# Performance work log

Hardware: AMD Instinct MI355X
Metric: run time of the kernel (lower is better)

## Reference

```python
import jax, jax.numpy as jnp
import numpy as np

N_NODES = 50000

def setup_inputs() -> dict:
    key = jax.random.key(0)
    k1, k2, k3, k4, k5, k6 = jax.random.split(key, 6)
    T, D, N, E = 10000, 128, N_NODES, 800000
    impact = jax.random.normal(k1, (T, D), dtype=jnp.float32)
    W = jax.random.normal(k2, (D, D), dtype=jnp.float32)
    M = jax.random.normal(k3, (D, D), dtype=jnp.float32)
    node_ids = jax.random.randint(k4, (N,), 0, T, dtype=jnp.int64)
    neighbor_ids = jax.random.randint(k5, (E,), 0, T, dtype=jnp.int64)
    neighbor_segments = jnp.sort(jax.random.randint(k6, (E,), 0, N, dtype=jnp.int64))
    return {"impact": impact, "W": W, "M": M, "node_ids": node_ids,
            "neighbor_ids": neighbor_ids, "neighbor_segments": neighbor_segments}

def reference(impact, W, M, node_ids, neighbor_ids, neighbor_segments):
    # Per node i (type k_i): s_i = relu(W @ h[k_i] + sum_{j in N(i)} M @ h[type_j])
    # result = softmax(sum_i s_i) over the D feature axis.
    self_feats = impact[node_ids]                          # (N, D) gather
    neigh_feats = impact[neighbor_ids]                     # (E, D) gather
    neigh_sum = jax.ops.segment_sum(neigh_feats, neighbor_segments,
                                    num_segments=N_NODES)  # (N, D) scatter-add
    pre = self_feats @ W.T + neigh_sum @ M.T               # (N, D)
    result = jnp.sum(jax.nn.relu(pre), axis=0)             # (D,)
    return jax.nn.softmax(result, axis=0)
```

## Files before the change

### kernel.cpp

```cpp
#include <hip/hip_runtime.h>
#include <hip/hip_fp16.h>

#define DDIM 128
#define ACC_BLOCKS 2048
#define NWALK (ACC_BLOCKS * 4)
#define RED_BLOCKS 64

typedef unsigned int uint;
typedef unsigned short ushort;
typedef __attribute__((ext_vector_type(8))) short bf16x8;
typedef __attribute__((ext_vector_type(4))) float f32x4;

static __device__ __forceinline__ ushort f2bf(float x) {
    uint u = __float_as_uint(x);
    u += 0x7fffu + ((u >> 16) & 1u);
    return (ushort)(u >> 16);
}

__global__ __launch_bounds__(256) void prep(
    const int* __restrict__ segs,
    const int* __restrict__ node_ids,
    const int* __restrict__ neighbor_ids,
    int* __restrict__ rowptr,
    int* __restrict__ items,
    int* __restrict__ done,
    int N, int E, int whoff, int mhoff)
{
    const int x = blockIdx.x * blockDim.x + threadIdx.x;
    if (x == 0) *done = 0;
    if (x >= E) return;

    const int sc = segs[x];
    const int sp = (x == 0) ? -1 : segs[x - 1];
    const int sn = (x + 1 < E) ? segs[x + 1] : N;

    items[x + sc + 1] = (mhoff + neighbor_ids[x] * 256) | ((sn != sc) ? (int)0x80000000 : 0);

    for (int i = sp + 1; i <= sc; ++i) {
        rowptr[i] = x;
        items[x + i] = (whoff + node_ids[i] * 256) | ((i < sc) ? (int)0x80000000 : 0);
    }
    if (x == E - 1) {
        for (int i = sc + 1; i <= N; ++i) {
            rowptr[i] = E;
            if (i < N) items[E + i] = (whoff + node_ids[i] * 256) | (int)0x80000000;
        }
#pragma unroll
        for (int q = 0; q < 32; ++q) items[N + E + q] = whoff;
    }
}

static __device__ __forceinline__ bf16x8 load_frag8(const float* base) {
    const float4 p = *reinterpret_cast<const float4*>(base);
    const float4 q = *reinterpret_cast<const float4*>(base + 4);
    bf16x8 f;
    f[0] = (short)f2bf(p.x); f[1] = (short)f2bf(p.y);
    f[2] = (short)f2bf(p.z); f[3] = (short)f2bf(p.w);
    f[4] = (short)f2bf(q.x); f[5] = (short)f2bf(q.y);
    f[6] = (short)f2bf(q.z); f[7] = (short)f2bf(q.w);
    return f;
}

__global__ __launch_bounds__(256) void precompute_mfma(
    const float* __restrict__ impact,
    const float* __restrict__ W,
    const float* __restrict__ Mm,
    __half* __restrict__ WhH,
    __half* __restrict__ MhH,
    const int* __restrict__ rowptr,
    int* __restrict__ wstart,
    int T, int N, int K)
{
    const int gid = blockIdx.x * 256 + threadIdx.x;
    if (gid <= NWALK) {
        const int t = (int)(((long long)gid * K) / NWALK);
        int lo = 0, hi = N;
        while (lo < hi) {
            const int mid = (lo + hi) >> 1;
            if (rowptr[mid] + mid < t) lo = mid + 1; else hi = mid;
        }
        wstart[gid] = rowptr[lo] + lo;
    }

    const int lane = threadIdx.x & 63;
    const int wv   = threadIdx.x >> 6;
    const int t0   = blockIdx.x * 32;
    const int r16  = lane & 15;
    const int kg   = lane >> 4;

    bf16x8 A[2][4];
#pragma unroll
    for (int rt = 0; rt < 2; ++rt) {
        int t = t0 + rt * 16 + r16;
        if (t >= T) t = T - 1;
        const float* abase = impact + (size_t)t * DDIM + kg * 8;
#pragma unroll
        for (int k0i = 0; k0i < 4; ++k0i)
            A[rt][k0i] = load_frag8(abase + k0i * 32);
    }

#pragma unroll
    for (int dti = 0; dti < 2; ++dti) {
        const int d0 = (wv * 2 + dti) * 16;
#pragma unroll
        for (int m = 0; m < 2; ++m) {
            const float* mat = (m == 0) ? W : Mm;
            __half* out = (m == 0) ? WhH : MhH;
            const float* bbase = mat + (size_t)(d0 + r16) * DDIM + kg * 8;
            f32x4 acc0 = {0.f, 0.f, 0.f, 0.f};
            f32x4 acc1 = {0.f, 0.f, 0.f, 0.f};
#pragma unroll
            for (int k0i = 0; k0i < 4; ++k0i) {
                const bf16x8 b = load_frag8(bbase + k0i * 32);
                acc0 = __builtin_amdgcn_mfma_f32_16x16x32_bf16(A[0][k0i], b, acc0, 0, 0, 0);
                acc1 = __builtin_amdgcn_mfma_f32_16x16x32_bf16(A[1][k0i], b, acc1, 0, 0, 0);
            }
            const int dcol = d0 + r16;
#pragma unroll
            for (int r = 0; r < 4; ++r) {
                const int tr0 = t0 + kg * 4 + r;
                const int tr1 = tr0 + 16;
                if (tr0 < T) out[(size_t)tr0 * DDIM + dcol] = __float2half(acc0[r]);
                if (tr1 < T) out[(size_t)tr1 * DDIM + dcol] = __float2half(acc1[r]);
            }
        }
    }
}

__global__ __launch_bounds__(256, 8) void accumulate_items(
    const char* __restrict__ tab,
    const int* __restrict__ items,
    const int* __restrict__ wstart,
    float* __restrict__ partials)
{
    const int lane = threadIdx.x & 63;
    const int wv   = __builtin_amdgcn_readfirstlane(threadIdx.x >> 6);
    const int w    = blockIdx.x * 4 + wv;

    const uint lb = (uint)lane << 2;

    const __half2 zero2 = __floats2half2_rn(0.f, 0.f);
    __half2 cc = zero2;
    float a0 = 0.f, a1 = 0.f;

    int k = __builtin_amdgcn_readfirstlane(wstart[w]);
    const int kend = __builtin_amdgcn_readfirstlane(wstart[w + 1]);

#define GATH(IW) (*reinterpret_cast<const __half2*>(tab + (((uint)(IW)) & 0x7fffffffu) + lb))
#define ACC(IW, V) { \
    cc = __hadd2(cc, V); \
    if ((IW) < 0) { \
        const float2 f = __half22float2(cc); \
        a0 += fmaxf(f.x, 0.f); a1 += fmaxf(f.y, 0.f); \
        cc = zero2; \
    } }
#define LOADI(Pa, Pb, Pc, Pd, kk) { \
    Pa = *reinterpret_cast<const int4*>(items + (kk)); \
    Pb = *reinterpret_cast<const int4*>(items + (kk) + 4); \
    Pc = *reinterpret_cast<const int4*>(items + (kk) + 8); \
    Pd = *reinterpret_cast<const int4*>(items + (kk) + 12); }
#define GATHER16(V, Pa, Pb, Pc, Pd) { \
    V[0] = GATH(Pa.x);  V[1] = GATH(Pa.y);  V[2]  = GATH(Pa.z);  V[3]  = GATH(Pa.w); \
    V[4] = GATH(Pb.x);  V[5] = GATH(Pb.y);  V[6]  = GATH(Pb.z);  V[7]  = GATH(Pb.w); \
    V[8] = GATH(Pc.x);  V[9] = GATH(Pc.y);  V[10] = GATH(Pc.z);  V[11] = GATH(Pc.w); \
    V[12] = GATH(Pd.x); V[13] = GATH(Pd.y); V[14] = GATH(Pd.z);  V[15] = GATH(Pd.w); }
#define ACC16(V, Pa, Pb, Pc, Pd) { \
    ACC(Pa.x, V[0]);  ACC(Pa.y, V[1]);  ACC(Pa.z, V[2]);   ACC(Pa.w, V[3]); \
    ACC(Pb.x, V[4]);  ACC(Pb.y, V[5]);  ACC(Pb.z, V[6]);   ACC(Pb.w, V[7]); \
    ACC(Pc.x, V[8]);  ACC(Pc.y, V[9]);  ACC(Pc.z, V[10]);  ACC(Pc.w, V[11]); \
    ACC(Pd.x, V[12]); ACC(Pd.y, V[13]); ACC(Pd.z, V[14]);  ACC(Pd.w, V[15]); }

    while (k < kend && (k & 15)) {
        const int iw = items[k];
        const __half2 v = GATH(iw);
        ACC(iw, v);
        ++k;
    }

    if (k + 32 <= kend) {
        int4 Aa, Ab, Ac, Ad, Ba, Bb, Bc, Bd;
        __half2 u[16], v[16];
        LOADI(Aa, Ab, Ac, Ad, k);
        GATHER16(u, Aa, Ab, Ac, Ad);
        LOADI(Ba, Bb, Bc, Bd, k + 16);
        k += 32;
        for (;;) {
            GATHER16(v, Ba, Bb, Bc, Bd);
            ACC16(u, Aa, Ab, Ac, Ad);
            if (k + 16 <= kend) { LOADI(Aa, Ab, Ac, Ad, k); k += 16; }
            else { ACC16(v, Ba, Bb, Bc, Bd); break; }
            GATHER16(u, Aa, Ab, Ac, Ad);
            ACC16(v, Ba, Bb, Bc, Bd);
            if (k + 16 <= kend) { LOADI(Ba, Bb, Bc, Bd, k); k += 16; }
            else { ACC16(u, Aa, Ab, Ac, Ad); break; }
        }
    }
    while (k < kend) {
        const int iw = items[k];
        const __half2 v = GATH(iw);
        ACC(iw, v);
        ++k;
    }

    {
        const float2 f = __half22float2(cc);
        a0 += fmaxf(f.x, 0.f);
        a1 += fmaxf(f.y, 0.f);
    }

    __shared__ float red[4][DDIM];
    red[wv][lane * 2 + 0] = a0;
    red[wv][lane * 2 + 1] = a1;
    __syncthreads();
    const int tid = threadIdx.x;
    if (tid < DDIM) {
        partials[(size_t)blockIdx.x * DDIM + tid] =
            red[0][tid] + red[1][tid] + red[2][tid] + red[3][tid];
    }
}

__global__ __launch_bounds__(256) void reduce_softmax(
    const float* __restrict__ partials, float* __restrict__ out2,
    float* __restrict__ out, int* __restrict__ done, int nb)
{
    const int tid = threadIdx.x;
    const int d = tid & (DDIM - 1);
    const int h = tid >> 7;
    {
        const int rows = nb / RED_BLOCKS;
        const int r0 = blockIdx.x * rows;
        float s = 0.f;
        for (int r = r0 + h; r < r0 + rows; r += 2)
            s += partials[(size_t)r * DDIM + d];
        __shared__ float red[2][DDIM];
        red[h][d] = s;
        __syncthreads();
        if (tid < DDIM)
            out2[(size_t)blockIdx.x * DDIM + tid] = red[0][tid] + red[1][tid];
    }
    __threadfence();
    __shared__ int isLast;
    if (tid == 0) {
        const int v = atomicAdd(done, 1);
        isLast = (v == RED_BLOCKS - 1) ? 1 : 0;
    }
    __syncthreads();
    if (!isLast) return;
    __threadfence();

    float s = 0.f;
    for (int b = h; b < RED_BLOCKS; b += 2)
        s += out2[(size_t)b * DDIM + d];
    __shared__ float r2[2][DDIM];
    r2[h][d] = s;
    __syncthreads();

    __shared__ float vec[DDIM];
    __shared__ float tmp[DDIM];
    if (tid < DDIM) { const float v = r2[0][tid] + r2[1][tid]; vec[tid] = v; tmp[tid] = v; }
    __syncthreads();
    for (int o = 64; o > 0; o >>= 1) {
        if (tid < o) tmp[tid] = fmaxf(tmp[tid], tmp[tid + o]);
        __syncthreads();
    }
    const float mx = tmp[0];
    __syncthreads();
    float ev = 0.f;
    if (tid < DDIM) { ev = expf(vec[tid] - mx); tmp[tid] = ev; }
    __syncthreads();
    for (int o = 64; o > 0; o >>= 1) {
        if (tid < o) tmp[tid] += tmp[tid + o];
        __syncthreads();
    }
    if (tid < DDIM) out[tid] = ev / tmp[0];
}

extern "C" void kernel_launch(void* const* d_in, const int* in_sizes, int n_in,
                              void* d_out, int out_size, void* d_ws, size_t ws_size,
                              hipStream_t stream) {
    const float* impact        = (const float*)d_in[0];
    const float* W             = (const float*)d_in[1];
    const float* Mm            = (const float*)d_in[2];
    const int*   node_ids      = (const int*)d_in[3];
    const int*   neighbor_ids  = (const int*)d_in[4];
    const int*   neighbor_segs = (const int*)d_in[5];

    const int T = in_sizes[0] / DDIM;
    const int N = in_sizes[3];
    const int E = in_sizes[4];
    const int K = N + E;

    char* ws = (char*)d_ws;
    size_t off = 0;
    const int whoff = (int)off;
    __half* WhH = (__half*)(ws + off);  off += (size_t)T * DDIM * sizeof(__half);
    const int mhoff = (int)off;
    __half* MhH = (__half*)(ws + off);  off += (size_t)T * DDIM * sizeof(__half);
    float* partials = (float*)(ws + off); off += (size_t)ACC_BLOCKS * DDIM * sizeof(float);
    float* part2    = (float*)(ws + off); off += (size_t)RED_BLOCKS * DDIM * sizeof(float);
    int*   rowptr   = (int*)(ws + off);   off += (size_t)(N + 1) * sizeof(int);
    int*   done     = (int*)(ws + off);   off += 256;
    off = (off + 255) & ~(size_t)255;
    int*   items    = (int*)(ws + off);   off += (size_t)(K + 32) * sizeof(int);
    int*   wstart   = (int*)(ws + off);   off += (size_t)(NWALK + 1) * sizeof(int);
    float* outf     = (float*)d_out;

    prep<<<(E + 255) / 256, 256, 0, stream>>>(
        neighbor_segs, node_ids, neighbor_ids, rowptr, items, done, N, E, whoff, mhoff);
    precompute_mfma<<<(T + 31) / 32, 256, 0, stream>>>(
        impact, W, Mm, WhH, MhH, rowptr, wstart, T, N, K);
    accumulate_items<<<ACC_BLOCKS, 256, 0, stream>>>(ws, items, wstart, partials);
    reduce_softmax<<<RED_BLOCKS, 256, 0, stream>>>(partials, part2, outf, done, ACC_BLOCKS);
}
```

Baseline: 62.02 us.

## Fuse prep and precompute kernels, derive walker starts from segments directly

Merges the CSR/item-list prep kernel and the MFMA precompute kernel into one launch, with extra blocks doing the prep work. Walker start positions are now found by binary search over the sorted segment array at edge-sampled points, so the rowptr array is no longer needed. This removes one kernel launch and the serial dependency on rowptr. In exchange the walker partition is sampled by edges rather than by items, which changes load balance slightly, and the two kinds of work now share one grid.

```diff
diff --git a/kernel.cpp b/kernel.cpp
--- a/kernel.cpp
+++ b/kernel.cpp
@@ -15,39 +15,6 @@
     uint u = __float_as_uint(x);
     u += 0x7fffu + ((u >> 16) & 1u);
     return (ushort)(u >> 16);
-}
-
-__global__ __launch_bounds__(256) void prep(
-    const int* __restrict__ segs,
-    const int* __restrict__ node_ids,
-    const int* __restrict__ neighbor_ids,
-    int* __restrict__ rowptr,
-    int* __restrict__ items,
-    int* __restrict__ done,
-    int N, int E, int whoff, int mhoff)
-{
-    const int x = blockIdx.x * blockDim.x + threadIdx.x;
-    if (x == 0) *done = 0;
-    if (x >= E) return;
-
-    const int sc = segs[x];
-    const int sp = (x == 0) ? -1 : segs[x - 1];
-    const int sn = (x + 1 < E) ? segs[x + 1] : N;
-
-    items[x + sc + 1] = (mhoff + neighbor_ids[x] * 256) | ((sn != sc) ? (int)0x80000000 : 0);
-
-    for (int i = sp + 1; i <= sc; ++i) {
-        rowptr[i] = x;
-        items[x + i] = (whoff + node_ids[i] * 256) | ((i < sc) ? (int)0x80000000 : 0);
-    }
-    if (x == E - 1) {
-        for (int i = sc + 1; i <= N; ++i) {
-            rowptr[i] = E;
-            if (i < N) items[E + i] = (whoff + node_ids[i] * 256) | (int)0x80000000;
-        }
-#pragma unroll
-        for (int q = 0; q < 32; ++q) items[N + E + q] = whoff;
-    }
 }
 
 static __device__ __forceinline__ bf16x8 load_frag8(const float* base) {
@@ -61,30 +28,68 @@
     return f;
 }
 
-__global__ __launch_bounds__(256) void precompute_mfma(
+__global__ __launch_bounds__(256) void fat_prep_precompute(
     const float* __restrict__ impact,
     const float* __restrict__ W,
     const float* __restrict__ Mm,
     __half* __restrict__ WhH,
     __half* __restrict__ MhH,
-    const int* __restrict__ rowptr,
+    const int* __restrict__ segs,
+    const int* __restrict__ node_ids,
+    const int* __restrict__ neighbor_ids,
+    int* __restrict__ items,
     int* __restrict__ wstart,
-    int T, int N, int K)
+    int* __restrict__ done,
+    int T, int N, int E, int PB, int whoff, int mhoff)
 {
-    const int gid = blockIdx.x * 256 + threadIdx.x;
-    if (gid <= NWALK) {
-        const int t = (int)(((long long)gid * K) / NWALK);
-        int lo = 0, hi = N;
-        while (lo < hi) {
-            const int mid = (lo + hi) >> 1;
-            if (rowptr[mid] + mid < t) lo = mid + 1; else hi = mid;
+    if ((int)blockIdx.x >= PB) {
+        const int x = ((int)blockIdx.x - PB) * 256 + (int)threadIdx.x;
+        const int K = N + E;
+        if (x == 0) *done = 0;
+
+        if (x < E) {
+            const int sc = segs[x];
+            const int sp = (x == 0) ? -1 : segs[x - 1];
+            const int sn = (x + 1 < E) ? segs[x + 1] : N;
+
+            items[x + sc + 1] = (mhoff + neighbor_ids[x] * 256)
+                              | ((sn != sc) ? (int)0x80000000 : 0);
+
+            for (int i = sp + 1; i <= sc; ++i)
+                items[x + i] = (whoff + node_ids[i] * 256)
+                             | ((i < sc) ? (int)0x80000000 : 0);
+
+            if (x == E - 1) {
+                for (int i = sc + 1; i < N; ++i)
+                    items[E + i] = (whoff + node_ids[i] * 256) | (int)0x80000000;
+#pragma unroll
+                for (int q = 0; q < 32; ++q) items[K + q] = whoff;
+            }
+        } else if (x <= E + NWALK) {
+            const int w = x - E;
+            int ws;
+            if (w == 0) ws = 0;
+            else {
+                const long long t = (long long)w * E / NWALK;
+                if (t >= E) ws = K;
+                else {
+                    const int n = segs[(int)t];
+                    int lo = 0, hi = (int)t;
+                    while (lo < hi) {
+                        const int mid = (lo + hi) >> 1;
+                        if (segs[mid] < n) lo = mid + 1; else hi = mid;
+                    }
+                    ws = lo + n;
+                }
+            }
+            wstart[w] = ws;
         }
-        wstart[gid] = rowptr[lo] + lo;
+        return;
     }
 
     const int lane = threadIdx.x & 63;
     const int wv   = threadIdx.x >> 6;
-    const int t0   = blockIdx.x * 32;
+    const int t0   = (int)blockIdx.x * 32;
     const int r16  = lane & 15;
     const int kg   = lane >> 4;
 
@@ -298,17 +303,18 @@
     __half* MhH = (__half*)(ws + off);  off += (size_t)T * DDIM * sizeof(__half);
     float* partials = (float*)(ws + off); off += (size_t)ACC_BLOCKS * DDIM * sizeof(float);
     float* part2    = (float*)(ws + off); off += (size_t)RED_BLOCKS * DDIM * sizeof(float);
-    int*   rowptr   = (int*)(ws + off);   off += (size_t)(N + 1) * sizeof(int);
     int*   done     = (int*)(ws + off);   off += 256;
     off = (off + 255) & ~(size_t)255;
     int*   items    = (int*)(ws + off);   off += (size_t)(K + 32) * sizeof(int);
     int*   wstart   = (int*)(ws + off);   off += (size_t)(NWALK + 1) * sizeof(int);
     float* outf     = (float*)d_out;
 
-    prep<<<(E + 255) / 256, 256, 0, stream>>>(
-        neighbor_segs, node_ids, neighbor_ids, rowptr, items, done, N, E, whoff, mhoff);
-    precompute_mfma<<<(T + 31) / 32, 256, 0, stream>>>(
-        impact, W, Mm, WhH, MhH, rowptr, wstart, T, N, K);
+    const int PB    = (T + 31) / 32;
+    const int PREPB = (E + NWALK + 1 + 255) / 256;
+
+    fat_prep_precompute<<<PB + PREPB, 256, 0, stream>>>(
+        impact, W, Mm, WhH, MhH, neighbor_segs, node_ids, neighbor_ids,
+        items, wstart, done, T, N, E, PB, whoff, mhoff);
     accumulate_items<<<ACC_BLOCKS, 256, 0, stream>>>(ws, items, wstart, partials);
     reduce_softmax<<<RED_BLOCKS, 256, 0, stream>>>(partials, part2, outf, done, ACC_BLOCKS);
 }
```

Measured after the change: 57.30 us. 7.6% less time.
